# Optimization experiments

Hardware: AMD Instinct MI355X
Metric: run time of the kernel (lower is better)

The kernel has to match this reference:

```python
import jax, jax.numpy as jnp
import numpy as np

MIN_DEPTH, MAX_DEPTH = 0.1, 100.0
BN_EPS = 1e-5


def _conv(x, w, b, pad):
    y = jax.lax.conv_general_dilated(
        x, w, window_strides=(1, 1), padding=[(pad, pad), (pad, pad)],
        dimension_numbers=("NCHW", "OIHW", "NCHW"))
    return y + b[None, :, None, None]


def _bn(x, gamma, beta, mean, var):
    # eval-mode BatchNorm2d with running stats
    inv = jax.lax.rsqrt(var + BN_EPS)
    return (x - mean[None, :, None, None]) * (gamma * inv)[None, :, None, None] + beta[None, :, None, None]


def _object_depths(depth, bboxes):
    # depth: (B,1,H,W), bboxes: (B,N,4) int — per-box median (lower median, like torch)
    B, _, H, W = depth.shape
    xs = jnp.arange(W)
    ys = jnp.arange(H)

    def per_image(d2, boxes):  # d2: (H,W), boxes: (N,4)
        dflat = d2.reshape(-1)

        def one_box(box):
            x1 = jnp.maximum(box[0], 0)
            y1 = jnp.maximum(box[1], 0)
            x2 = jnp.minimum(box[2], W)
            y2 = jnp.minimum(box[3], H)
            mask = (((ys >= y1) & (ys < y2))[:, None] & ((xs >= x1) & (xs < x2))[None, :]).reshape(-1)
            vals = jnp.where(mask, dflat, jnp.inf)
            s = jnp.sort(vals)
            k = mask.sum()
            idx = jnp.maximum((k - 1) // 2, 0)
            med = jnp.take(s, idx)
            return jnp.where(k > 0, med, jnp.zeros((), dtype=d2.dtype))

        return jax.vmap(one_box)(boxes)

    return jax.vmap(per_image)(depth[:, 0], bboxes)


def _forward(features, bboxes, w1, b1, g1, be1, m1, v1, w2, b2, g2, be2, m2, v2,
             w3, b3, uw1, ub1, uw2, ub2):
    # depth head
    h = jax.nn.relu(_bn(_conv(features, w1, b1, 1), g1, be1, m1, v1))
    h = jax.nn.relu(_bn(_conv(h, w2, b2, 1), g2, be2, m2, v2))
    disp = jax.nn.sigmoid(_conv(h, w3, b3, 0))  # (B,1,H,W)
    min_disp = 1.0 / MAX_DEPTH
    max_disp = 1.0 / MIN_DEPTH
    depth = 1.0 / (min_disp + (max_disp - min_disp) * disp)
    # uncertainty head
    u = jax.nn.relu(_conv(features, uw1, ub1, 1))
    uncertainty = jax.nn.softplus(_conv(u, uw2, ub2, 0))
    obj = _object_depths(depth, bboxes)
    return depth, uncertainty, obj


def setup_inputs() -> dict:
    key = jax.random.key(0)
    ks = jax.random.split(key, 16)
    B, C, Hc, H, W, N = 8, 256, 256, 96, 160, 64
    f32 = jnp.float32
    inp = {
        "features": jax.random.normal(ks[0], (B, C, H, W), dtype=f32),
        "bboxes": jax.random.randint(ks[1], (B, N, 4), 0, 96, dtype=jnp.int32),
        "w1": jax.random.normal(ks[2], (Hc, C, 3, 3), dtype=f32) * 0.02,
        "b1": jnp.zeros((Hc,), f32),
        "g1": jnp.ones((Hc,), f32),
        "be1": jnp.zeros((Hc,), f32),
        "m1": jax.random.normal(ks[3], (Hc,), dtype=f32) * 0.1,
        "v1": jnp.ones((Hc,), f32),
        "w2": jax.random.normal(ks[4], (Hc, Hc, 3, 3), dtype=f32) * 0.02,
        "b2": jnp.zeros((Hc,), f32),
        "g2": jnp.ones((Hc,), f32),
        "be2": jnp.zeros((Hc,), f32),
        "m2": jax.random.normal(ks[5], (Hc,), dtype=f32) * 0.1,
        "v2": jnp.ones((Hc,), f32),
        "w3": jax.random.normal(ks[6], (1, Hc, 1, 1), dtype=f32) * 0.05,
        "b3": jnp.zeros((1,), f32),
        "uw1": jax.random.normal(ks[7], (Hc // 2, C, 3, 3), dtype=f32) * 0.02,
        "ub1": jnp.zeros((Hc // 2,), f32),
        "uw2": jax.random.normal(ks[8], (1, Hc // 2, 1, 1), dtype=f32) * 0.05,
        "ub2": jnp.zeros((1,), f32),
    }
    return inp


def reference(features, bboxes, w1, b1, g1, be1, m1, v1, w2, b2, g2, be2, m2, v2,
              w3, b3, uw1, ub1, uw2, ub2):
    return _forward(features, bboxes, w1, b1, g1, be1, m1, v1, w2, b2, g2, be2,
                    m2, v2, w3, b3, uw1, ub1, uw2, ub2)
```

## Files before the change

### kernel.cpp

```cpp
#include <hip/hip_runtime.h>
#include <hip/hip_bf16.h>

#define HH 96
#define WW 160
#define BATCH 8
#define NPIX (BATCH*HH*WW)
#define CIN 256
#define IMG (HH*WW)
#define PW 162
#define PH 98
#define PR (PH*PW)
#define PTOT (BATCH*PR)

typedef short bf16x8 __attribute__((ext_vector_type(8)));
typedef float f32x4 __attribute__((ext_vector_type(4)));

__device__ __forceinline__ unsigned short f2bf(float f) {
    unsigned int u = __float_as_uint(f);
    u = (u + 0x7fffu + ((u >> 16) & 1u)) >> 16;
    return (unsigned short)u;
}

__device__ __forceinline__ void gload16(const void* g, void* l) {
    __builtin_amdgcn_global_load_lds(
        (const __attribute__((address_space(1))) void*)g,
        (__attribute__((address_space(3))) void*)l,
        16, 0, 0);
}

__global__ __launch_bounds__(256) void prep_all(
    const float* __restrict__ w1, const float* __restrict__ w2, const float* __restrict__ uw1,
    unsigned short* __restrict__ w1T, unsigned short* __restrict__ w2T, unsigned short* __restrict__ uw1T,
    unsigned int* __restrict__ featPu, unsigned int* __restrict__ h1Pu, float* __restrict__ outd,
    const float* __restrict__ b1, const float* __restrict__ g1, const float* __restrict__ be1,
    const float* __restrict__ m1, const float* __restrict__ v1,
    const float* __restrict__ b2, const float* __restrict__ g2, const float* __restrict__ be2,
    const float* __restrict__ m2, const float* __restrict__ v2,
    const float* __restrict__ ub1,
    float* __restrict__ scale1, float* __restrict__ bias1,
    float* __restrict__ scale2, float* __restrict__ bias2,
    const float* __restrict__ f, unsigned short* __restrict__ ft)
{
    __shared__ float tile[32][33];
    const int bid = blockIdx.x;
    const int t = threadIdx.x;

    if (bid < 5760) {
        const int S = 256 * 2304;
        int i = bid * 256 + t;
        if (i < S) {
            int co = i / 2304, r = i % 2304, pos = r >> 8, ci = r & 255;
            w1T[i] = f2bf(w1[(co * 256 + ci) * 9 + pos]);
        } else if (i < 2 * S) {
            int j = i - S;
            int co = j / 2304, r = j % 2304, pos = r >> 8, ci = r & 255;
            w2T[j] = f2bf(w2[(co * 256 + ci) * 9 + pos]);
        } else {
            int j = i - 2 * S;
            int co = j / 2304, r = j % 2304, pos = r >> 8, ci = r & 255;
            uw1T[j] = f2bf(uw1[(co * 256 + ci) * 9 + pos]);
        }
    } else if (bid < 9888) {
        int k2 = (bid - 5760) * 2 + (t >> 7);
        int lane = t & 127;
        unsigned int* buf = (k2 < 4128) ? featPu : h1Pu;
        int k = (k2 < 4128) ? k2 : (k2 - 4128);
        int img = k / 516, i = k % 516;
        int py, px;
        if (i < PW)            { py = 0;      px = i; }
        else if (i < 2 * PW)   { py = PH - 1; px = i - PW; }
        else { int q = i - 2 * PW; py = 1 + (q >> 1); px = (q & 1) ? (PW - 1) : 0; }
        size_t row = (size_t)img * PR + (size_t)py * PW + px;
        buf[row * 128 + lane] = 0;
    } else if (bid < 10368) {
        outd[(size_t)(bid - 9888) * 256 + t] = 0.f;
    } else if (bid == 10368) {
        if (t < 256) {
            float s1 = g1[t] * rsqrtf(v1[t] + 1e-5f);
            scale1[t] = s1;
            bias1[t]  = (b1[t] - m1[t]) * s1 + be1[t];
            float s2 = g2[t] * rsqrtf(v2[t] + 1e-5f);
            scale2[t] = s2;
            bias2[t]  = (b2[t] - m2[t]) * s2 + be2[t];
            if (t < 128) { scale1[256 + t] = 1.0f; bias1[256 + t] = ub1[t]; }
        }
    } else {
        int id = bid - 10369;
        int x0 = (id % 5) * 32;
        int c0 = ((id / 5) % 8) * 32;
        int by = id / 40;
        int b = by / HH, y = by % HH;
        int tx = t & 31, tg = t >> 5;
        const float* src = f + (((size_t)(b * CIN + c0) * HH + y) * WW) + x0;
        #pragma unroll
        for (int i = 0; i < 4; ++i) {
            int cl = tg + i * 8;
            tile[cl][tx] = src[(size_t)cl * HH * WW + tx];
        }
        __syncthreads();
        size_t rbase = (size_t)b * PR + (size_t)(y + 1) * PW + (x0 + 1);
        #pragma unroll
        for (int i = 0; i < 4; ++i) {
            int xl = tg + i * 8;
            ft[(rbase + xl) * 256 + c0 + tx] = f2bf(tile[tx][xl]);
        }
    }
}

__global__ __launch_bounds__(256, 2) void conv3x3_mfma(
    const unsigned short* __restrict__ inP,
    const unsigned short* __restrict__ wT,
    const float* __restrict__ scale, const float* __restrict__ bias,
    unsigned short* __restrict__ outT,
    float* __restrict__ uout,
    const float* __restrict__ uw2, const float* __restrict__ ub2,
    int Cout, int mode, int My)
{
    __shared__ unsigned short Alds[3 * 128 * 32];
    __shared__ unsigned short Blds[272 * 32];
    __shared__ float usum[2][256];

    const int t = threadIdx.x;
    const int wave = t >> 6;
    const int l = t & 63;

    const int lid = blockIdx.x;
    const int xcd = lid & 7;
    const int j = lid >> 3;
    const int n0 = (xcd * 60 + j / My) * 256;
    const int m0 = (j % My) * 128;
    const bool is_unc = (mode == 1) && (m0 == 256);

    const int b0 = n0 / IMG;
    const int rem0 = n0 % IMG;
    const int y0 = rem0 / WW;
    const int x0 = rem0 % WW;
    const int r0 = b0 * PR + (y0 + 1) * PW + (x0 + 1);

    const int lrow = l >> 2;
    const int lkq = (l & 3) ^ ((l >> 3) & 3);

    const unsigned short* asrc0 = wT + (size_t)(m0 + wave * 32 + lrow) * 9 * 256 + lkq * 8;
    const unsigned short* asrc1 = asrc0 + (size_t)16 * 9 * 256;

    char* AldsB = (char*)Alds;
    char* BldsB = (char*)Blds;
    char* aldst = AldsB + wave * 2048;

    const int wm = wave >> 1, wn = wave & 1;
    const int quad = l >> 4, lane16 = l & 15;
    const int aoff = lane16 * 64 + ((quad ^ ((lane16 >> 1) & 3)) << 4);

    int browbase[8];
    #pragma unroll
    for (int i = 0; i < 8; ++i) {
        int jj = wn * 128 + i * 16 + lane16;
        browbase[i] = jj + 2 * ((x0 + jj) / WW) + 7;
    }

    f32x4 acc[4][8];
    #pragma unroll
    for (int mt = 0; mt < 4; ++mt)
        #pragma unroll
        for (int nt = 0; nt < 8; ++nt)
            acc[mt][nt] = (f32x4){0.f, 0.f, 0.f, 0.f};

    for (int cc = 0; cc < 8; ++cc) {
        const int ccoff = cc * 32;
        for (int dyi = 0; dyi < 3; ++dyi) {
            __syncthreads();
            const unsigned short* a0 = asrc0 + (dyi * 3) * 256 + ccoff;
            const unsigned short* a1 = asrc1 + (dyi * 3) * 256 + ccoff;
            #pragma unroll
            for (int dxp = 0; dxp < 3; ++dxp) {
                gload16(a0 + dxp * 256, aldst + dxp * 8192);
                gload16(a1 + dxp * 256, aldst + dxp * 8192 + 1024);
            }
            const ptrdiff_t rs = (ptrdiff_t)r0 + (ptrdiff_t)(dyi - 1) * PW - 8;
            const unsigned short* bs0 = inP + (rs + lrow) * 256 + ccoff + lkq * 8;
            #pragma unroll
            for (int k = 0; k < 4; ++k) {
                const int s = wave * 4 + k;
                gload16(bs0 + s * 4096, BldsB + s * 1024);
            }
            if (wave == 3) gload16(bs0 + 16 * 4096, BldsB + 16 * 1024);
            __syncthreads();
            #pragma unroll
            for (int dx = 0; dx < 3; ++dx) {
                bf16x8 af[4], bfr[8];
                #pragma unroll
                for (int mt = 0; mt < 4; ++mt)
                    af[mt] = *(const bf16x8*)(AldsB + dx * 8192 + ((wm * 4 + mt) << 10) + aoff);
                #pragma unroll
                for (int i = 0; i < 8; ++i) {
                    int row = browbase[i] + dx;
                    int ba = (row << 6) + ((quad ^ ((row >> 1) & 3)) << 4);
                    bfr[i] = *(const bf16x8*)(BldsB + ba);
                }
                #pragma unroll
                for (int mt = 0; mt < 4; ++mt)
                    #pragma unroll
                    for (int nt = 0; nt < 8; ++nt)
                        acc[mt][nt] = __builtin_amdgcn_mfma_f32_16x16x32_bf16(
                            af[mt], bfr[nt], acc[mt][nt], 0, 0, 0);
            }
        }
    }

    if (is_unc) {
        const float* ub = bias + 256;
        float s[8] = {0.f, 0.f, 0.f, 0.f, 0.f, 0.f, 0.f, 0.f};
        #pragma unroll
        for (int mt = 0; mt < 4; ++mt) {
            const int mg = wm * 64 + mt * 16 + quad * 4;
            const float4 bi = *(const float4*)&ub[mg];
            const float4 uw = *(const float4*)&uw2[mg];
            #pragma unroll
            for (int nt = 0; nt < 8; ++nt) {
                s[nt] += fmaxf(acc[mt][nt][0] + bi.x, 0.f) * uw.x
                       + fmaxf(acc[mt][nt][1] + bi.y, 0.f) * uw.y
                       + fmaxf(acc[mt][nt][2] + bi.z, 0.f) * uw.z
                       + fmaxf(acc[mt][nt][3] + bi.w, 0.f) * uw.w;
            }
        }
        #pragma unroll
        for (int nt = 0; nt < 8; ++nt) {
            s[nt] += __shfl_xor(s[nt], 16);
            s[nt] += __shfl_xor(s[nt], 32);
        }
        if (quad == 0) {
            #pragma unroll
            for (int nt = 0; nt < 8; ++nt)
                usum[wm][wn * 128 + nt * 16 + lane16] = s[nt];
        }
        __syncthreads();
        {
            float x = usum[0][t] + usum[1][t] + ub2[0];
            uout[n0 + t] = fmaxf(x, 0.f) + log1pf(expf(-fabsf(x)));
        }
        return;
    }

    if (mode == 0) {
        float s[8] = {0.f, 0.f, 0.f, 0.f, 0.f, 0.f, 0.f, 0.f};
        #pragma unroll
        for (int mt = 0; mt < 4; ++mt) {
            const int mg = m0 + wm * 64 + mt * 16 + quad * 4;
            const float4 sc = *(const float4*)&scale[mg];
            const float4 bi = *(const float4*)&bias[mg];
            const float4 w  = *(const float4*)&uw2[mg];
            #pragma unroll
            for (int nt = 0; nt < 8; ++nt) {
                s[nt] += fmaxf(acc[mt][nt][0] * sc.x + bi.x, 0.f) * w.x
                       + fmaxf(acc[mt][nt][1] * sc.y + bi.y, 0.f) * w.y
                       + fmaxf(acc[mt][nt][2] * sc.z + bi.z, 0.f) * w.z
                       + fmaxf(acc[mt][nt][3] * sc.w + bi.w, 0.f) * w.w;
            }
        }
        #pragma unroll
        for (int nt = 0; nt < 8; ++nt) {
            s[nt] += __shfl_xor(s[nt], 16);
            s[nt] += __shfl_xor(s[nt], 32);
        }
        if (quad == 0) {
            #pragma unroll
            for (int nt = 0; nt < 8; ++nt)
                usum[wm][wn * 128 + nt * 16 + lane16] = s[nt];
        }
        __syncthreads();
        atomicAdd(&uout[n0 + t], usum[0][t] + usum[1][t]);
        return;
    }

    size_t obase[8];
    #pragma unroll
    for (int nt = 0; nt < 8; ++nt) {
        int n = n0 + wn * 128 + nt * 16 + lane16;
        int b = n / IMG, rem = n % IMG, yy = rem / WW, xx = rem % WW;
        obase[nt] = ((size_t)(b * PH + yy + 1) * PW + (xx + 1)) * 256;
    }
    #pragma unroll
    for (int mt = 0; mt < 4; ++mt) {
        const int mg = m0 + wm * 64 + mt * 16 + quad * 4;
        const float4 sc = *(const float4*)&scale[mg];
        const float4 bi = *(const float4*)&bias[mg];
        #pragma unroll
        for (int nt = 0; nt < 8; ++nt) {
            ushort4 pk;
            pk.x = f2bf(fmaxf(acc[mt][nt][0] * sc.x + bi.x, 0.f));
            pk.y = f2bf(fmaxf(acc[mt][nt][1] * sc.y + bi.y, 0.f));
            pk.z = f2bf(fmaxf(acc[mt][nt][2] * sc.z + bi.z, 0.f));
            pk.w = f2bf(fmaxf(acc[mt][nt][3] * sc.w + bi.w, 0.f));
            *(ushort4*)&outT[obase[nt] + mg] = pk;
        }
    }
}

__global__ __launch_bounds__(256) void depth_transform(
    float* __restrict__ out, const float* __restrict__ b3)
{
    int i = blockIdx.x * 256 + threadIdx.x;
    float x = out[i] + b3[0];
    float sig = 1.f / (1.f + expf(-x));
    out[i] = 1.f / (0.01f + 9.99f * sig);
}

__global__ __launch_bounds__(256) void median_kernel(
    const float* __restrict__ depth, const int* __restrict__ bboxes, float* __restrict__ obj)
{
    const int bi = blockIdx.x;
    const int b = bi >> 6;
    const int* bb = bboxes + (size_t)bi * 4;
    int x1 = max(bb[0], 0), y1 = max(bb[1], 0);
    int x2 = min(bb[2], WW), y2 = min(bb[3], HH);
    int w = x2 - x1, h = y2 - y1;
    if (w <= 0 || h <= 0) {
        if (threadIdx.x == 0) obj[bi] = 0.f;
        return;
    }
    const int wh = w * h;
    int tgt = (wh - 1) >> 1;
    const float* dbase = depth + (size_t)b * HH * WW;

    __shared__ unsigned int hist[256];
    __shared__ unsigned int sel_prefix, sel_target;
    unsigned int prefix = 0;

    for (int pass = 0; pass < 4; ++pass) {
        const int shift = 24 - 8 * pass;
        hist[threadIdx.x] = 0;
        __syncthreads();
        const unsigned int mask_high = (pass == 0) ? 0u : (0xFFFFFFFFu << (shift + 8));
        for (int idx = threadIdx.x; idx < wh; idx += 256) {
            int yy = y1 + idx / w, xx = x1 + idx % w;
            unsigned int uu = __float_as_uint(dbase[yy * WW + xx]);
            if ((uu & mask_high) == (prefix & mask_high))
                atomicAdd(&hist[(uu >> shift) & 255], 1u);
        }
        __syncthreads();
        if (threadIdx.x == 0) {
            unsigned int cum = 0;
            for (int bin = 0; bin < 256; ++bin) {
                unsigned int c = hist[bin];
                if (cum + c > (unsigned int)tgt) {
                    sel_target = (unsigned int)tgt - cum;
                    sel_prefix = prefix | ((unsigned int)bin << shift);
                    break;
                }
                cum += c;
            }
        }
        __syncthreads();
        prefix = sel_prefix;
        tgt = (int)sel_target;
    }
    if (threadIdx.x == 0) obj[bi] = __uint_as_float(prefix);
}

extern "C" void kernel_launch(void* const* d_in, const int* in_sizes, int n_in,
                              void* d_out, int out_size, void* d_ws, size_t ws_size,
                              hipStream_t stream) {
    const float* features = (const float*)d_in[0];
    const int*   bboxes   = (const int*)d_in[1];
    const float* w1  = (const float*)d_in[2];
    const float* b1  = (const float*)d_in[3];
    const float* g1  = (const float*)d_in[4];
    const float* be1 = (const float*)d_in[5];
    const float* m1  = (const float*)d_in[6];
    const float* v1  = (const float*)d_in[7];
    const float* w2  = (const float*)d_in[8];
    const float* b2  = (const float*)d_in[9];
    const float* g2  = (const float*)d_in[10];
    const float* be2 = (const float*)d_in[11];
    const float* m2  = (const float*)d_in[12];
    const float* v2  = (const float*)d_in[13];
    const float* w3  = (const float*)d_in[14];
    const float* b3  = (const float*)d_in[15];
    const float* uw1 = (const float*)d_in[16];
    const float* ub1 = (const float*)d_in[17];
    const float* uw2 = (const float*)d_in[18];
    const float* ub2 = (const float*)d_in[19];
    float* out = (float*)d_out;

    char* ws = (char*)d_ws;
    unsigned short* featP = (unsigned short*)(ws + 8192);
    unsigned short* h1P   = (unsigned short*)(ws + 65044480);
    unsigned short* w1T   = (unsigned short*)(ws + 130080768);
    unsigned short* uw1T  = w1T + 256 * 2304;
    unsigned short* w2T   = uw1T + 128 * 2304;
    float* scale1 = (float*)(w2T + 589824);
    float* bias1  = scale1 + 384;
    float* scale2 = bias1 + 384;
    float* bias2  = scale2 + 256;

    prep_all<<<41089, 256, 0, stream>>>(
        w1, w2, uw1, w1T, w2T, uw1T,
        (unsigned int*)featP, (unsigned int*)h1P, out,
        b1, g1, be1, m1, v1, b2, g2, be2, m2, v2, ub1,
        scale1, bias1, scale2, bias2,
        features, featP);

    conv3x3_mfma<<<1440, 256, 0, stream>>>(
        featP, w1T, scale1, bias1, h1P, out + NPIX, uw2, ub2, 256, 1, 3);
    conv3x3_mfma<<<960, 256, 0, stream>>>(
        h1P, w2T, scale2, bias2, nullptr, out, w3, nullptr, 256, 0, 2);

    depth_transform<<<NPIX / 256, 256, 0, stream>>>(out, b3);
    median_kernel<<<BATCH * 64, 256, 0, stream>>>(out, bboxes, out + 2 * NPIX);
}
```

Before: 604.9 us.

## Double-buffer B tile and software-pipeline A/B loads across dx phases

```diff
diff --git a/kernel.cpp b/kernel.cpp
--- a/kernel.cpp
+++ b/kernel.cpp
@@ -117,7 +117,7 @@
     int Cout, int mode, int My)
 {
     __shared__ unsigned short Alds[3 * 128 * 32];
-    __shared__ unsigned short Blds[272 * 32];
+    __shared__ unsigned short Blds[2][272 * 32];
     __shared__ float usum[2][256];
 
     const int t = threadIdx.x;
@@ -165,47 +165,94 @@
         for (int nt = 0; nt < 8; ++nt)
             acc[mt][nt] = (f32x4){0.f, 0.f, 0.f, 0.f};
 
-    for (int cc = 0; cc < 8; ++cc) {
-        const int ccoff = cc * 32;
-        for (int dyi = 0; dyi < 3; ++dyi) {
-            __syncthreads();
-            const unsigned short* a0 = asrc0 + (dyi * 3) * 256 + ccoff;
-            const unsigned short* a1 = asrc1 + (dyi * 3) * 256 + ccoff;
-            #pragma unroll
-            for (int dxp = 0; dxp < 3; ++dxp) {
-                gload16(a0 + dxp * 256, aldst + dxp * 8192);
-                gload16(a1 + dxp * 256, aldst + dxp * 8192 + 1024);
-            }
-            const ptrdiff_t rs = (ptrdiff_t)r0 + (ptrdiff_t)(dyi - 1) * PW - 8;
-            const unsigned short* bs0 = inP + (rs + lrow) * 256 + ccoff + lkq * 8;
-            #pragma unroll
-            for (int k = 0; k < 4; ++k) {
-                const int s = wave * 4 + k;
-                gload16(bs0 + s * 4096, BldsB + s * 1024);
-            }
-            if (wave == 3) gload16(bs0 + 16 * 4096, BldsB + 16 * 1024);
-            __syncthreads();
-            #pragma unroll
-            for (int dx = 0; dx < 3; ++dx) {
-                bf16x8 af[4], bfr[8];
-                #pragma unroll
-                for (int mt = 0; mt < 4; ++mt)
-                    af[mt] = *(const bf16x8*)(AldsB + dx * 8192 + ((wm * 4 + mt) << 10) + aoff);
-                #pragma unroll
-                for (int i = 0; i < 8; ++i) {
-                    int row = browbase[i] + dx;
-                    int ba = (row << 6) + ((quad ^ ((row >> 1) & 3)) << 4);
-                    bfr[i] = *(const bf16x8*)(BldsB + ba);
-                }
-                #pragma unroll
-                for (int mt = 0; mt < 4; ++mt)
-                    #pragma unroll
-                    for (int nt = 0; nt < 8; ++nt)
-                        acc[mt][nt] = __builtin_amdgcn_mfma_f32_16x16x32_bf16(
-                            af[mt], bfr[nt], acc[mt][nt], 0, 0, 0);
-            }
-        }
-    }
+    auto STAGE_B = [&](int ccoff, int dyi, int sel) {
+        const ptrdiff_t rs = (ptrdiff_t)r0 + (ptrdiff_t)(dyi - 1) * PW - 8;
+        const unsigned short* bs0 = inP + (rs + lrow) * 256 + ccoff + lkq * 8;
+        char* bd = BldsB + sel * 17408;
+        #pragma unroll
+        for (int k = 0; k < 4; ++k) {
+            const int s = wave * 4 + k;
+            gload16(bs0 + s * 4096, bd + s * 1024);
+        }
+        if (wave == 3) gload16(bs0 + 16 * 4096, bd + 16 * 1024);
+    };
+    auto STAGE_A = [&](int ccoff, int pos, int slot) {
+        const unsigned short* a0 = asrc0 + pos * 256 + ccoff;
+        const unsigned short* a1 = asrc1 + pos * 256 + ccoff;
+        gload16(a0, aldst + slot * 8192);
+        gload16(a1, aldst + slot * 8192 + 1024);
+    };
+
+    STAGE_B(0, 0, 0);
+    STAGE_A(0, 0, 0);
+    STAGE_A(0, 1, 1);
+    asm volatile("s_waitcnt vmcnt(0)" ::: "memory");
+    __builtin_amdgcn_s_barrier();
+    asm volatile("" ::: "memory");
+
+    #define COMPUTE_PHASE(d)                                                          \
+    {                                                                                 \
+        __builtin_amdgcn_s_setprio(1);                                                \
+        bf16x8 af[4], bfr[8];                                                         \
+        _Pragma("unroll")                                                             \
+        for (int mt = 0; mt < 4; ++mt)                                                \
+            af[mt] = *(const bf16x8*)(AldsB + (d) * 8192 + ((wm * 4 + mt) << 10) + aoff); \
+        _Pragma("unroll")                                                             \
+        for (int i = 0; i < 8; ++i) {                                                 \
+            int row = browbase[i] + (d);                                              \
+            int ba = (row << 6) + ((quad ^ ((row >> 1) & 3)) << 4);                   \
+            bfr[i] = *(const bf16x8*)(Bb + ba);                                       \
+        }                                                                             \
+        _Pragma("unroll")                                                             \
+        for (int mt = 0; mt < 4; ++mt)                                                \
+            _Pragma("unroll")                                                         \
+            for (int nt = 0; nt < 8; ++nt)                                            \
+                acc[mt][nt] = __builtin_amdgcn_mfma_f32_16x16x32_bf16(                \
+                    af[mt], bfr[nt], acc[mt][nt], 0, 0, 0);                           \
+        __builtin_amdgcn_s_setprio(0);                                                \
+    }
+
+    for (int it = 0; it < 24; ++it) {
+        const int dyi = it - (it / 3) * 3;
+        const int ccoff = (it / 3) * 32;
+        const int itn = it + 1;
+        const int dyin = itn - (itn / 3) * 3;
+        const int ccoffn = (itn / 3) * 32;
+        const char* Bb = BldsB + (it & 1) * 17408;
+
+        asm volatile("s_waitcnt vmcnt(2)" ::: "memory");
+        __builtin_amdgcn_sched_barrier(0);
+        __builtin_amdgcn_s_barrier();
+        asm volatile("" ::: "memory");
+        STAGE_A(ccoff, dyi * 3 + 2, 2);
+        if (it < 23) STAGE_B(ccoffn, dyin, itn & 1);
+        COMPUTE_PHASE(0);
+
+        if (it < 23) {
+            if (wave == 3) { asm volatile("s_waitcnt vmcnt(7)" ::: "memory"); }
+            else           { asm volatile("s_waitcnt vmcnt(6)" ::: "memory"); }
+        } else {
+            asm volatile("s_waitcnt vmcnt(2)" ::: "memory");
+        }
+        __builtin_amdgcn_sched_barrier(0);
+        __builtin_amdgcn_s_barrier();
+        asm volatile("" ::: "memory");
+        if (it < 23) STAGE_A(ccoffn, dyin * 3 + 0, 0);
+        COMPUTE_PHASE(1);
+
+        if (it < 23) {
+            if (wave == 3) { asm volatile("s_waitcnt vmcnt(7)" ::: "memory"); }
+            else           { asm volatile("s_waitcnt vmcnt(6)" ::: "memory"); }
+        } else {
+            asm volatile("s_waitcnt vmcnt(0)" ::: "memory");
+        }
+        __builtin_amdgcn_sched_barrier(0);
+        __builtin_amdgcn_s_barrier();
+        asm volatile("" ::: "memory");
+        if (it < 23) STAGE_A(ccoffn, dyin * 3 + 1, 1);
+        COMPUTE_PHASE(2);
+    }
+    #undef COMPUTE_PHASE
 
     if (is_unc) {
         const float* ub = bias + 256;
@@ -228,6 +275,7 @@
             s[nt] += __shfl_xor(s[nt], 16);
             s[nt] += __shfl_xor(s[nt], 32);
         }
+        __syncthreads();
         if (quad == 0) {
             #pragma unroll
             for (int nt = 0; nt < 8; ++nt)
@@ -262,6 +310,7 @@
             s[nt] += __shfl_xor(s[nt], 16);
             s[nt] += __shfl_xor(s[nt], 32);
         }
+        __syncthreads();
         if (quad == 0) {
             #pragma unroll
             for (int nt = 0; nt < 8; ++nt)
```

Result: no change. 602.3 us (-0.4%).
